# Kernel tuning notes

Measured on AMD Instinct MI355X. Metric: run time of the kernel, lower is better.

## Reference

```python
import jax, jax.numpy as jnp
import numpy as np

E = 512
H = 8
HD = E // H
EPS = 1e-5


def setup_inputs() -> dict:
    key = jax.random.key(0)
    ks = jax.random.split(key, 12)
    S, B = 2048, 4
    bound_in = float(np.sqrt(6.0 / (3 * E + E)))  # xavier_uniform for in_proj
    inp = {
        "x": jax.random.normal(ks[0], (S, B, E), dtype=jnp.float32),
        "in_proj_weight": jax.random.uniform(ks[1], (3 * E, E), minval=-bound_in, maxval=bound_in, dtype=jnp.float32),
        "in_proj_bias": jnp.zeros((3 * E,), jnp.float32),
        "out_proj_weight": jax.random.normal(ks[2], (E, E), dtype=jnp.float32) * 0.02,
        "out_proj_bias": jnp.zeros((E,), jnp.float32),
        "ln1_gamma": jnp.ones((E,), jnp.float32),
        "ln1_beta": jnp.zeros((E,), jnp.float32),
        "fc1_weight": jax.random.normal(ks[3], (4 * E, E), dtype=jnp.float32) * 0.02,
        "fc1_bias": jnp.zeros((4 * E,), jnp.float32),
        "fc2_weight": jax.random.normal(ks[4], (E, 4 * E), dtype=jnp.float32) * 0.02,
        "fc2_bias": jnp.zeros((E,), jnp.float32),
        "ln2_gamma": jnp.ones((E,), jnp.float32),
        "ln2_beta": jnp.zeros((E,), jnp.float32),
    }
    return inp


def _layer_norm(x, gamma, beta):
    mu = jnp.mean(x, axis=-1, keepdims=True)
    var = jnp.mean(jnp.square(x - mu), axis=-1, keepdims=True)
    return (x - mu) * jax.lax.rsqrt(var + EPS) * gamma + beta


def _encoder_layer(x, in_w, in_b, out_w, out_b, g1, b1, fc1_w, fc1_b, fc2_w, fc2_b, g2, b2):
    S, B, _ = x.shape
    # --- self attention (hand-rolled, full S x S scores as in original) ---
    qkv = x @ in_w.T + in_b                      # [S, B, 3E]
    q, k, v = jnp.split(qkv, 3, axis=-1)         # each [S, B, E]
    # [S, B, E] -> [B*H, S, HD]
    def to_heads(t):
        return t.reshape(S, B * H, HD).transpose(1, 0, 2)
    q, k, v = to_heads(q), to_heads(k), to_heads(v)
    scores = jnp.einsum('bsd,btd->bst', q, k) / jnp.sqrt(jnp.float32(HD))  # [B*H, S, S]
    attn_w = jax.nn.softmax(scores, axis=-1)
    attn = jnp.einsum('bst,btd->bsd', attn_w, v)  # [B*H, S, HD]
    attn = attn.transpose(1, 0, 2).reshape(S, B, E)
    attn = attn @ out_w.T + out_b
    # --- residual + LN ---
    x = _layer_norm(x + attn, g1, b1)
    # --- FFN ---
    h = jax.nn.relu(x @ fc1_w.T + fc1_b)
    h = h @ fc2_w.T + fc2_b
    return _layer_norm(x + h, g2, b2)


def reference(x, in_proj_weight, in_proj_bias, out_proj_weight, out_proj_bias,
              ln1_gamma, ln1_beta, fc1_weight, fc1_bias, fc2_weight, fc2_bias,
              ln2_gamma, ln2_beta):
    return _encoder_layer(x, in_proj_weight, in_proj_bias, out_proj_weight, out_proj_bias,
                          ln1_gamma, ln1_beta, fc1_weight, fc1_bias, fc2_weight, fc2_bias,
                          ln2_gamma, ln2_beta)
```

## Files before the change

kernel.cpp:

```cpp
#include <hip/hip_runtime.h>

typedef _Float16 half8 __attribute__((ext_vector_type(8)));
typedef float f32x4 __attribute__((ext_vector_type(4)));

static __device__ __forceinline__ f32x4 mfma16(half8 a, half8 b, f32x4 c) {
    return __builtin_amdgcn_mfma_f32_16x16x32_f16(a, b, c, 0, 0, 0);
}

__global__ void __launch_bounds__(256) f32_to_f16(const float* __restrict__ in,
                                                  _Float16* __restrict__ out, int n) {
    long i = ((long)blockIdx.x * 256 + threadIdx.x) * 8;
    if (i >= n) return;
    f32x4 v0 = *(const f32x4*)(in + i);
    f32x4 v1 = *(const f32x4*)(in + i + 4);
    half8 h;
#pragma unroll
    for (int j = 0; j < 4; j++) { h[j] = (_Float16)v0[j]; h[4 + j] = (_Float16)v1[j]; }
    *(half8*)(out + i) = h;
}

template <int MODE>
__global__ void __launch_bounds__(256) gemm_bt(const _Float16* __restrict__ A,
                                               const _Float16* __restrict__ Bw,
                                               const float* __restrict__ bias,
                                               const float* __restrict__ resid,
                                               void* __restrict__ Cout,
                                               int M, int N, int K) {
    __shared__ __align__(16) _Float16 As[128 * 32];
    __shared__ __align__(16) _Float16 Bs[128 * 32];
    const int tid = threadIdx.x;
    const int lane = tid & 63;
    const int w = tid >> 6;
    const int g = lane >> 4, l15 = lane & 15;
    const int wm = w >> 1, wn = w & 1;
    const long rowblk = (long)blockIdx.y * 128;
    const long colblk = (long)blockIdx.x * 128;

    const int srow = tid >> 2;
    const int scol = (tid & 3) * 8;
    const _Float16* Ap = A + (rowblk + srow) * (long)K + scol;
    const _Float16* Bp = Bw + (colblk + srow) * (long)K + scol;
    const long halfK = 64L * K;

    f32x4 zero = {0.f, 0.f, 0.f, 0.f};
    f32x4 acc[4][4];
#pragma unroll
    for (int i = 0; i < 4; i++)
#pragma unroll
        for (int j = 0; j < 4; j++) acc[i][j] = zero;

    for (int k0 = 0; k0 < K; k0 += 32) {
        half8 a1 = *(const half8*)(Ap + k0);
        half8 a2 = *(const half8*)(Ap + halfK + k0);
        half8 b1 = *(const half8*)(Bp + k0);
        half8 b2 = *(const half8*)(Bp + halfK + k0);
        __syncthreads();
        *(half8*)(As + tid * 8) = a1;
        *(half8*)(As + 2048 + tid * 8) = a2;
        *(half8*)(Bs + tid * 8) = b1;
        *(half8*)(Bs + 2048 + tid * 8) = b2;
        __syncthreads();
        half8 af[4], bf[4];
#pragma unroll
        for (int mi = 0; mi < 4; mi++)
            af[mi] = *(const half8*)(As + (wm * 64 + mi * 16 + l15) * 32 + g * 8);
#pragma unroll
        for (int ni = 0; ni < 4; ni++)
            bf[ni] = *(const half8*)(Bs + (wn * 64 + ni * 16 + l15) * 32 + g * 8);
#pragma unroll
        for (int mi = 0; mi < 4; mi++)
#pragma unroll
            for (int ni = 0; ni < 4; ni++)
                acc[mi][ni] = mfma16(af[mi], bf[ni], acc[mi][ni]);
    }

    const long crow0 = rowblk + wm * 64 + g * 4;
    const long ccol0 = colblk + wn * 64 + l15;
#pragma unroll
    for (int mi = 0; mi < 4; mi++) {
#pragma unroll
        for (int ni = 0; ni < 4; ni++) {
            const long cc = ccol0 + ni * 16;
            const float bv = bias[cc];
#pragma unroll
            for (int r = 0; r < 4; r++) {
                const long rr = crow0 + mi * 16 + r;
                float v = acc[mi][ni][r] + bv;
                if (MODE == 1) v = fmaxf(v, 0.f);
                if (MODE == 2) {
                    ((float*)Cout)[rr * N + cc] = v + resid[rr * N + cc];
                } else {
                    ((_Float16*)Cout)[rr * N + cc] = (_Float16)v;
                }
            }
        }
    }
}

__global__ void __launch_bounds__(256) build_vt(const _Float16* __restrict__ qkv,
                                                _Float16* __restrict__ vt) {
    const int tid = threadIdx.x, lane = tid & 63, w = tid >> 6;
    const int bh = blockIdx.y, b = bh >> 3, h = bh & 7;
    const int tc = blockIdx.x * 4 + w;
    const int d = lane;
#pragma unroll
    for (int jj = 0; jj < 8; jj++) {
        half8 buf;
#pragma unroll
        for (int j = 0; j < 8; j++) {
            int t = tc * 64 + jj * 8 + j;
            buf[j] = qkv[(long)(t * 4 + b) * 1536 + 1024 + h * 64 + d];
        }
        *(half8*)(vt + (long)(bh * 64 + d) * 2048 + tc * 64 + jj * 8) = buf;
    }
}

__global__ void __launch_bounds__(256) attn_fwd(const _Float16* __restrict__ qkv,
                                                const _Float16* __restrict__ vt,
                                                _Float16* __restrict__ attn_out) {
    __shared__ __align__(16) _Float16 Plds[4][32 * 72];
    const int tid = threadIdx.x;
    const int lane = tid & 63;
    const int w = tid >> 6;
    const int g = lane >> 4, l15 = lane & 15;
    const int bh = blockIdx.y;
    const int b = bh >> 3, h = bh & 7;
    const int s0 = blockIdx.x * 128 + w * 32;
    const int qoff = h * 64;

    half8 qa[2][2];
#pragma unroll
    for (int mi = 0; mi < 2; mi++)
#pragma unroll
        for (int ks = 0; ks < 2; ks++) {
            long row = (long)((s0 + mi * 16 + l15) * 4 + b) * 1536;
            qa[mi][ks] = *(const half8*)(qkv + row + qoff + ks * 32 + g * 8);
        }

    f32x4 zero = {0.f, 0.f, 0.f, 0.f};
    f32x4 o[2][4];
    float mst[2][4], lst[2][4];
#pragma unroll
    for (int mi = 0; mi < 2; mi++) {
#pragma unroll
        for (int di = 0; di < 4; di++) o[mi][di] = zero;
#pragma unroll
        for (int r = 0; r < 4; r++) { mst[mi][r] = -1e30f; lst[mi][r] = 0.f; }
    }

    for (int t0 = 0; t0 < 2048; t0 += 64) {
        f32x4 sa[2][4];
#pragma unroll
        for (int mi = 0; mi < 2; mi++)
#pragma unroll
            for (int ni = 0; ni < 4; ni++) sa[mi][ni] = zero;

#pragma unroll
        for (int ni = 0; ni < 4; ni++)
#pragma unroll
            for (int ks = 0; ks < 2; ks++) {
                long row = (long)((t0 + ni * 16 + l15) * 4 + b) * 1536;
                half8 kb = *(const half8*)(qkv + row + 512 + qoff + ks * 32 + g * 8);
                sa[0][ni] = mfma16(qa[0][ks], kb, sa[0][ni]);
                sa[1][ni] = mfma16(qa[1][ks], kb, sa[1][ni]);
            }

#pragma unroll
        for (int mi = 0; mi < 2; mi++)
#pragma unroll
            for (int ni = 0; ni < 4; ni++)
#pragma unroll
                for (int r = 0; r < 4; r++) sa[mi][ni][r] *= 0.125f;

        float corr[2][4];
#pragma unroll
        for (int mi = 0; mi < 2; mi++)
#pragma unroll
            for (int r = 0; r < 4; r++) {
                float mx = fmaxf(fmaxf(sa[mi][0][r], sa[mi][1][r]),
                                 fmaxf(sa[mi][2][r], sa[mi][3][r]));
                mx = fmaxf(mx, __shfl_xor(mx, 1));
                mx = fmaxf(mx, __shfl_xor(mx, 2));
                mx = fmaxf(mx, __shfl_xor(mx, 4));
                mx = fmaxf(mx, __shfl_xor(mx, 8));
                float mnew = fmaxf(mst[mi][r], mx);
                float c = __expf(mst[mi][r] - mnew);
                corr[mi][r] = c;
                mst[mi][r] = mnew;
                float rs = 0.f;
#pragma unroll
                for (int ni = 0; ni < 4; ni++) {
                    float p = __expf(sa[mi][ni][r] - mnew);
                    sa[mi][ni][r] = p;
                    rs += p;
                }
                rs += __shfl_xor(rs, 1);
                rs += __shfl_xor(rs, 2);
                rs += __shfl_xor(rs, 4);
                rs += __shfl_xor(rs, 8);
                lst[mi][r] = lst[mi][r] * c + rs;
                const int prow = mi * 16 + g * 4 + r;
#pragma unroll
                for (int ni = 0; ni < 4; ni++)
                    Plds[w][prow * 72 + ni * 16 + l15] = (_Float16)sa[mi][ni][r];
            }

#pragma unroll
        for (int mi = 0; mi < 2; mi++)
#pragma unroll
            for (int di = 0; di < 4; di++)
#pragma unroll
                for (int r = 0; r < 4; r++) o[mi][di][r] *= corr[mi][r];

        half8 pa[2][2];
#pragma unroll
        for (int mi = 0; mi < 2; mi++)
#pragma unroll
            for (int ks = 0; ks < 2; ks++)
                pa[mi][ks] = *(const half8*)&Plds[w][(mi * 16 + l15) * 72 + ks * 32 + g * 8];
#pragma unroll
        for (int di = 0; di < 4; di++)
#pragma unroll
            for (int ks = 0; ks < 2; ks++) {
                long vrow = (long)(bh * 64 + di * 16 + l15) * 2048;
                half8 vb = *(const half8*)(vt + vrow + t0 + ks * 32 + g * 8);
                o[0][di] = mfma16(pa[0][ks], vb, o[0][di]);
                o[1][di] = mfma16(pa[1][ks], vb, o[1][di]);
            }
    }

#pragma unroll
    for (int mi = 0; mi < 2; mi++)
#pragma unroll
        for (int r = 0; r < 4; r++) {
            float inv = 1.f / lst[mi][r];
            long srow = (long)((s0 + mi * 16 + g * 4 + r) * 4 + b) * 512;
#pragma unroll
            for (int di = 0; di < 4; di++)
                attn_out[srow + qoff + di * 16 + l15] = (_Float16)(o[mi][di][r] * inv);
        }
}

__global__ void __launch_bounds__(256) ln_rows(const float* __restrict__ in,
                                               const float* __restrict__ gamma,
                                               const float* __restrict__ beta,
                                               float* __restrict__ outf,
                                               _Float16* __restrict__ outh) {
    const int tid = threadIdx.x, lane = tid & 63, w = tid >> 6;
    const long row = (long)blockIdx.x * 4 + w;
    const float* p = in + row * 512 + lane * 8;
    f32x4 v0 = *(const f32x4*)p;
    f32x4 v1 = *(const f32x4*)(p + 4);
    float s = v0[0] + v0[1] + v0[2] + v0[3] + v1[0] + v1[1] + v1[2] + v1[3];
    float q = v0[0] * v0[0] + v0[1] * v0[1] + v0[2] * v0[2] + v0[3] * v0[3] +
              v1[0] * v1[0] + v1[1] * v1[1] + v1[2] * v1[2] + v1[3] * v1[3];
#pragma unroll
    for (int off = 1; off < 64; off <<= 1) {
        s += __shfl_xor(s, off);
        q += __shfl_xor(q, off);
    }
    const float mu = s * (1.0f / 512.0f);
    const float var = q * (1.0f / 512.0f) - mu * mu;
    const float rstd = rsqrtf(var + 1e-5f);
    const float* gp = gamma + lane * 8;
    const float* bp = beta + lane * 8;
    f32x4 g0 = *(const f32x4*)gp, g1 = *(const f32x4*)(gp + 4);
    f32x4 b0 = *(const f32x4*)bp, b1 = *(const f32x4*)(bp + 4);
    f32x4 o0, o1;
#pragma unroll
    for (int j = 0; j < 4; j++) {
        o0[j] = (v0[j] - mu) * rstd * g0[j] + b0[j];
        o1[j] = (v1[j] - mu) * rstd * g1[j] + b1[j];
    }
    float* op = outf + row * 512 + lane * 8;
    *(f32x4*)op = o0;
    *(f32x4*)(op + 4) = o1;
    if (outh) {
        half8 h;
#pragma unroll
        for (int j = 0; j < 4; j++) { h[j] = (_Float16)o0[j]; h[4 + j] = (_Float16)o1[j]; }
        *(half8*)(outh + row * 512 + lane * 8) = h;
    }
}

extern "C" void kernel_launch(void* const* d_in, const int* in_sizes, int n_in,
                              void* d_out, int out_size, void* d_ws, size_t ws_size,
                              hipStream_t stream) {
    const float* x    = (const float*)d_in[0];
    const float* inw  = (const float*)d_in[1];
    const float* inb  = (const float*)d_in[2];
    const float* outw = (const float*)d_in[3];
    const float* outb = (const float*)d_in[4];
    const float* g1   = (const float*)d_in[5];
    const float* b1   = (const float*)d_in[6];
    const float* f1w  = (const float*)d_in[7];
    const float* f1b  = (const float*)d_in[8];
    const float* f2w  = (const float*)d_in[9];
    const float* f2b  = (const float*)d_in[10];
    const float* g2   = (const float*)d_in[11];
    const float* b2   = (const float*)d_in[12];

    char* ws = (char*)d_ws;
    const long MB = 1024 * 1024;
    _Float16* X16  = (_Float16*)(ws + 0);
    _Float16* QKV  = (_Float16*)(ws + 8 * MB);
    _Float16* H16  = (_Float16*)(ws + 0);
    _Float16* VT   = (_Float16*)(ws + 32 * MB);
    _Float16* ATT  = (_Float16*)(ws + 40 * MB);
    float*    PRE  = (float*)(ws + 48 * MB);
    float*    YF   = (float*)(ws + 64 * MB);
    _Float16* Y16  = (_Float16*)(ws + 80 * MB);
    _Float16* WIN  = (_Float16*)(ws + 88 * MB);
    _Float16* WOUT = (_Float16*)(ws + 90 * MB);
    _Float16* WF1  = (_Float16*)(ws + 91 * MB);
    _Float16* WF2  = (_Float16*)(ws + 93 * MB);

    f32_to_f16<<<2048, 256, 0, stream>>>(x, X16, 8192 * 512);
    f32_to_f16<<<384, 256, 0, stream>>>(inw, WIN, 1536 * 512);
    f32_to_f16<<<128, 256, 0, stream>>>(outw, WOUT, 512 * 512);
    f32_to_f16<<<512, 256, 0, stream>>>(f1w, WF1, 2048 * 512);
    f32_to_f16<<<512, 256, 0, stream>>>(f2w, WF2, 512 * 2048);

    gemm_bt<0><<<dim3(12, 64), 256, 0, stream>>>(X16, WIN, inb, nullptr, QKV, 8192, 1536, 512);
    build_vt<<<dim3(8, 32), 256, 0, stream>>>(QKV, VT);
    attn_fwd<<<dim3(16, 32), 256, 0, stream>>>(QKV, VT, ATT);
    gemm_bt<2><<<dim3(4, 64), 256, 0, stream>>>(ATT, WOUT, outb, x, PRE, 8192, 512, 512);
    ln_rows<<<2048, 256, 0, stream>>>(PRE, g1, b1, YF, Y16);
    gemm_bt<1><<<dim3(16, 64), 256, 0, stream>>>(Y16, WF1, f1b, nullptr, H16, 8192, 2048, 512);
    gemm_bt<2><<<dim3(4, 64), 256, 0, stream>>>(H16, WF2, f2b, YF, PRE, 8192, 512, 2048);
    ln_rows<<<2048, 256, 0, stream>>>(PRE, g2, b2, (float*)d_out, nullptr);
}
```

Before: 360.3 us.

## Write QKV head-major, use direct-to-LDS GEMM loads, shrink attention and N=512 tiles

The QKV projection epilogue now scatters Q, K and V into contiguous per-head [B*H, S, 64] buffers. A shared-memory tiled transpose builds V^T, and attention reads contiguous head rows instead of strided 1536-wide rows. GEMM tile loads now use global_load_lds to bypass registers. A template parameter gives the N=512 GEMMs 64-wide tiles for more blocks. Attention uses 16 query rows per wave with twice as many blocks, and the softmax scale is folded into the exp. Risks are scattered 2-byte stores in the QKV epilogue and the loss of K/V register reuse across two query tiles.

```diff
diff --git a/kernel.cpp b/kernel.cpp
--- a/kernel.cpp
+++ b/kernel.cpp
@@ -5,6 +5,13 @@
 
 static __device__ __forceinline__ f32x4 mfma16(half8 a, half8 b, f32x4 c) {
     return __builtin_amdgcn_mfma_f32_16x16x32_f16(a, b, c, 0, 0, 0);
+}
+
+static __device__ __forceinline__ void gload16(const void* g, const void* l) {
+    __builtin_amdgcn_global_load_lds(
+        (const __attribute__((address_space(1))) unsigned int*)(unsigned long long)g,
+        (__attribute__((address_space(3))) unsigned int*)(unsigned int)(unsigned long long)l,
+        16, 0, 0);
 }
 
 __global__ void __launch_bounds__(256) f32_to_f16(const float* __restrict__ in,
@@ -19,67 +26,63 @@
     *(half8*)(out + i) = h;
 }
 
-template <int MODE>
+template <int MODE, int NI>
 __global__ void __launch_bounds__(256) gemm_bt(const _Float16* __restrict__ A,
                                                const _Float16* __restrict__ Bw,
                                                const float* __restrict__ bias,
                                                const float* __restrict__ resid,
                                                void* __restrict__ Cout,
                                                int M, int N, int K) {
+    constexpr int BN = 32 * NI;
     __shared__ __align__(16) _Float16 As[128 * 32];
-    __shared__ __align__(16) _Float16 Bs[128 * 32];
+    __shared__ __align__(16) _Float16 Bs[BN * 32];
     const int tid = threadIdx.x;
     const int lane = tid & 63;
     const int w = tid >> 6;
     const int g = lane >> 4, l15 = lane & 15;
     const int wm = w >> 1, wn = w & 1;
     const long rowblk = (long)blockIdx.y * 128;
-    const long colblk = (long)blockIdx.x * 128;
-
-    const int srow = tid >> 2;
-    const int scol = (tid & 3) * 8;
-    const _Float16* Ap = A + (rowblk + srow) * (long)K + scol;
-    const _Float16* Bp = Bw + (colblk + srow) * (long)K + scol;
-    const long halfK = 64L * K;
+    const long colblk = (long)blockIdx.x * BN;
+
+    const int lrow = lane >> 2;
+    const int lcol = (lane & 3) * 8;
 
     f32x4 zero = {0.f, 0.f, 0.f, 0.f};
-    f32x4 acc[4][4];
+    f32x4 acc[4][NI];
 #pragma unroll
     for (int i = 0; i < 4; i++)
 #pragma unroll
-        for (int j = 0; j < 4; j++) acc[i][j] = zero;
+        for (int j = 0; j < NI; j++) acc[i][j] = zero;
 
     for (int k0 = 0; k0 < K; k0 += 32) {
-        half8 a1 = *(const half8*)(Ap + k0);
-        half8 a2 = *(const half8*)(Ap + halfK + k0);
-        half8 b1 = *(const half8*)(Bp + k0);
-        half8 b2 = *(const half8*)(Bp + halfK + k0);
         __syncthreads();
-        *(half8*)(As + tid * 8) = a1;
-        *(half8*)(As + 2048 + tid * 8) = a2;
-        *(half8*)(Bs + tid * 8) = b1;
-        *(half8*)(Bs + 2048 + tid * 8) = b2;
+        gload16(A + (rowblk + w * 32 + lrow) * (long)K + k0 + lcol, As + w * 1024);
+        gload16(A + (rowblk + w * 32 + 16 + lrow) * (long)K + k0 + lcol, As + w * 1024 + 512);
+#pragma unroll
+        for (int c = 0; c < NI / 2; c++)
+            gload16(Bw + (colblk + w * (8 * NI) + c * 16 + lrow) * (long)K + k0 + lcol,
+                    Bs + w * (8 * NI) * 32 + c * 512);
         __syncthreads();
-        half8 af[4], bf[4];
+        half8 af[4], bf[NI];
 #pragma unroll
         for (int mi = 0; mi < 4; mi++)
             af[mi] = *(const half8*)(As + (wm * 64 + mi * 16 + l15) * 32 + g * 8);
 #pragma unroll
-        for (int ni = 0; ni < 4; ni++)
-            bf[ni] = *(const half8*)(Bs + (wn * 64 + ni * 16 + l15) * 32 + g * 8);
+        for (int ni = 0; ni < NI; ni++)
+            bf[ni] = *(const half8*)(Bs + (wn * (16 * NI) + ni * 16 + l15) * 32 + g * 8);
 #pragma unroll
         for (int mi = 0; mi < 4; mi++)
 #pragma unroll
-            for (int ni = 0; ni < 4; ni++)
+            for (int ni = 0; ni < NI; ni++)
                 acc[mi][ni] = mfma16(af[mi], bf[ni], acc[mi][ni]);
     }
 
     const long crow0 = rowblk + wm * 64 + g * 4;
-    const long ccol0 = colblk + wn * 64 + l15;
+    const long ccol0 = colblk + wn * (16 * NI) + l15;
 #pragma unroll
     for (int mi = 0; mi < 4; mi++) {
 #pragma unroll
-        for (int ni = 0; ni < 4; ni++) {
+        for (int ni = 0; ni < NI; ni++) {
             const long cc = ccol0 + ni * 16;
             const float bv = bias[cc];
 #pragma unroll
@@ -89,6 +92,13 @@
                 if (MODE == 1) v = fmaxf(v, 0.f);
                 if (MODE == 2) {
                     ((float*)Cout)[rr * N + cc] = v + resid[rr * N + cc];
+                } else if (MODE == 3) {
+                    const long sel = cc >> 9;
+                    const int hh = (int)(cc >> 6) & 7;
+                    const int dd = (int)cc & 63;
+                    const int ss = (int)(rr >> 2), bb = (int)rr & 3;
+                    ((_Float16*)Cout)[sel * (32L * 2048 * 64) +
+                                      ((long)(bb * 8 + hh) * 2048 + ss) * 64 + dd] = (_Float16)v;
                 } else {
                     ((_Float16*)Cout)[rr * N + cc] = (_Float16)v;
                 }
@@ -97,148 +107,122 @@
     }
 }
 
-__global__ void __launch_bounds__(256) build_vt(const _Float16* __restrict__ qkv,
-                                                _Float16* __restrict__ vt) {
-    const int tid = threadIdx.x, lane = tid & 63, w = tid >> 6;
-    const int bh = blockIdx.y, b = bh >> 3, h = bh & 7;
-    const int tc = blockIdx.x * 4 + w;
-    const int d = lane;
-#pragma unroll
-    for (int jj = 0; jj < 8; jj++) {
-        half8 buf;
-#pragma unroll
-        for (int j = 0; j < 8; j++) {
-            int t = tc * 64 + jj * 8 + j;
-            buf[j] = qkv[(long)(t * 4 + b) * 1536 + 1024 + h * 64 + d];
-        }
-        *(half8*)(vt + (long)(bh * 64 + d) * 2048 + tc * 64 + jj * 8) = buf;
-    }
-}
-
-__global__ void __launch_bounds__(256) attn_fwd(const _Float16* __restrict__ qkv,
-                                                const _Float16* __restrict__ vt,
-                                                _Float16* __restrict__ attn_out) {
-    __shared__ __align__(16) _Float16 Plds[4][32 * 72];
+__global__ void __launch_bounds__(256) transpose_v(const _Float16* __restrict__ Vh,
+                                                   _Float16* __restrict__ Vt) {
+    __shared__ _Float16 T[64][72];
+    const int tid = threadIdx.x;
+    const int bh = blockIdx.y;
+    const int t0 = blockIdx.x * 64;
+    const _Float16* src = Vh + ((long)bh * 2048 + t0) * 64;
+    const int row = tid >> 2, col = (tid & 3) * 16;
+    *(half8*)&T[row][col] = *(const half8*)(src + row * 64 + col);
+    *(half8*)&T[row][col + 8] = *(const half8*)(src + row * 64 + col + 8);
+    __syncthreads();
+    const int d = tid >> 2, tc = (tid & 3) * 16;
+    half8 a, b;
+#pragma unroll
+    for (int j = 0; j < 8; j++) { a[j] = T[tc + j][d]; b[j] = T[tc + 8 + j][d]; }
+    _Float16* dst = Vt + ((long)bh * 64 + d) * 2048 + t0 + tc;
+    *(half8*)dst = a;
+    *(half8*)(dst + 8) = b;
+}
+
+__global__ void __launch_bounds__(256) attn_fwd(const _Float16* __restrict__ Qh,
+                                                const _Float16* __restrict__ Kh,
+                                                const _Float16* __restrict__ Vt,
+                                                _Float16* __restrict__ out) {
+    __shared__ __align__(16) _Float16 Plds[4][16 * 72];
     const int tid = threadIdx.x;
     const int lane = tid & 63;
     const int w = tid >> 6;
     const int g = lane >> 4, l15 = lane & 15;
     const int bh = blockIdx.y;
     const int b = bh >> 3, h = bh & 7;
-    const int s0 = blockIdx.x * 128 + w * 32;
-    const int qoff = h * 64;
-
-    half8 qa[2][2];
-#pragma unroll
-    for (int mi = 0; mi < 2; mi++)
-#pragma unroll
-        for (int ks = 0; ks < 2; ks++) {
-            long row = (long)((s0 + mi * 16 + l15) * 4 + b) * 1536;
-            qa[mi][ks] = *(const half8*)(qkv + row + qoff + ks * 32 + g * 8);
+    const int s0 = blockIdx.x * 64 + w * 16;
+    const _Float16* Qb = Qh + (long)bh * 2048 * 64;
+    const _Float16* Kb = Kh + (long)bh * 2048 * 64;
+    const _Float16* Vb = Vt + (long)bh * 64 * 2048;
+
+    half8 qa[2];
+#pragma unroll
+    for (int ks = 0; ks < 2; ks++)
+        qa[ks] = *(const half8*)(Qb + (s0 + l15) * 64 + ks * 32 + g * 8);
+
+    f32x4 zero = {0.f, 0.f, 0.f, 0.f};
+    f32x4 o[4];
+    float mst[4], lst[4];
+#pragma unroll
+    for (int di = 0; di < 4; di++) o[di] = zero;
+#pragma unroll
+    for (int r = 0; r < 4; r++) { mst[r] = -1e30f; lst[r] = 0.f; }
+
+    for (int t0 = 0; t0 < 2048; t0 += 64) {
+        f32x4 sa[4];
+#pragma unroll
+        for (int ni = 0; ni < 4; ni++) sa[ni] = zero;
+#pragma unroll
+        for (int ni = 0; ni < 4; ni++)
+#pragma unroll
+            for (int ks = 0; ks < 2; ks++) {
+                half8 kb = *(const half8*)(Kb + (t0 + ni * 16 + l15) * 64 + ks * 32 + g * 8);
+                sa[ni] = mfma16(qa[ks], kb, sa[ni]);
+            }
+
+        float corr[4];
+#pragma unroll
+        for (int r = 0; r < 4; r++) {
+            float mx = fmaxf(fmaxf(sa[0][r], sa[1][r]), fmaxf(sa[2][r], sa[3][r]));
+            mx = fmaxf(mx, __shfl_xor(mx, 1));
+            mx = fmaxf(mx, __shfl_xor(mx, 2));
+            mx = fmaxf(mx, __shfl_xor(mx, 4));
+            mx = fmaxf(mx, __shfl_xor(mx, 8));
+            const float mnew = fmaxf(mst[r], mx);
+            corr[r] = __expf((mst[r] - mnew) * 0.125f);
+            mst[r] = mnew;
+            float rs = 0.f;
+            float pv[4];
+#pragma unroll
+            for (int ni = 0; ni < 4; ni++) {
+                pv[ni] = __expf((sa[ni][r] - mnew) * 0.125f);
+                rs += pv[ni];
+            }
+            rs += __shfl_xor(rs, 1);
+            rs += __shfl_xor(rs, 2);
+            rs += __shfl_xor(rs, 4);
+            rs += __shfl_xor(rs, 8);
+            lst[r] = lst[r] * corr[r] + rs;
+            const int prow = g * 4 + r;
+#pragma unroll
+            for (int ni = 0; ni < 4; ni++)
+                Plds[w][prow * 72 + ni * 16 + l15] = (_Float16)pv[ni];
         }
 
-    f32x4 zero = {0.f, 0.f, 0.f, 0.f};
-    f32x4 o[2][4];
-    float mst[2][4], lst[2][4];
-#pragma unroll
-    for (int mi = 0; mi < 2; mi++) {
-#pragma unroll
-        for (int di = 0; di < 4; di++) o[mi][di] = zero;
-#pragma unroll
-        for (int r = 0; r < 4; r++) { mst[mi][r] = -1e30f; lst[mi][r] = 0.f; }
-    }
-
-    for (int t0 = 0; t0 < 2048; t0 += 64) {
-        f32x4 sa[2][4];
-#pragma unroll
-        for (int mi = 0; mi < 2; mi++)
-#pragma unroll
-            for (int ni = 0; ni < 4; ni++) sa[mi][ni] = zero;
-
-#pragma unroll
-        for (int ni = 0; ni < 4; ni++)
+#pragma unroll
+        for (int di = 0; di < 4; di++)
+#pragma unroll
+            for (int r = 0; r < 4; r++) o[di][r] *= corr[r];
+
+        half8 pa[2];
+#pragma unroll
+        for (int ks = 0; ks < 2; ks++)
+            pa[ks] = *(const half8*)&Plds[w][l15 * 72 + ks * 32 + g * 8];
+#pragma unroll
+        for (int di = 0; di < 4; di++)
 #pragma unroll
             for (int ks = 0; ks < 2; ks++) {
-                long row = (long)((t0 + ni * 16 + l15) * 4 + b) * 1536;
-                half8 kb = *(const half8*)(qkv + row + 512 + qoff + ks * 32 + g * 8);
-                sa[0][ni] = mfma16(qa[0][ks], kb, sa[0][ni]);
-                sa[1][ni] = mfma16(qa[1][ks], kb, sa[1][ni]);
+                half8 vb = *(const half8*)(Vb + (di * 16 + l15) * 2048 + t0 + ks * 32 + g * 8);
+                o[di] = mfma16(pa[ks], vb, o[di]);
             }
-
-#pragma unroll
-        for (int mi = 0; mi < 2; mi++)
-#pragma unroll
-            for (int ni = 0; ni < 4; ni++)
-#pragma unroll
-                for (int r = 0; r < 4; r++) sa[mi][ni][r] *= 0.125f;
-
-        float corr[2][4];
-#pragma unroll
-        for (int mi = 0; mi < 2; mi++)
-#pragma unroll
-            for (int r = 0; r < 4; r++) {
-                float mx = fmaxf(fmaxf(sa[mi][0][r], sa[mi][1][r]),
-                                 fmaxf(sa[mi][2][r], sa[mi][3][r]));
-                mx = fmaxf(mx, __shfl_xor(mx, 1));
-                mx = fmaxf(mx, __shfl_xor(mx, 2));
-                mx = fmaxf(mx, __shfl_xor(mx, 4));
-                mx = fmaxf(mx, __shfl_xor(mx, 8));
-                float mnew = fmaxf(mst[mi][r], mx);
-                float c = __expf(mst[mi][r] - mnew);
-                corr[mi][r] = c;
-                mst[mi][r] = mnew;
-                float rs = 0.f;
-#pragma unroll
-                for (int ni = 0; ni < 4; ni++) {
-                    float p = __expf(sa[mi][ni][r] - mnew);
-                    sa[mi][ni][r] = p;
-                    rs += p;
-                }
-                rs += __shfl_xor(rs, 1);
-                rs += __shfl_xor(rs, 2);
-                rs += __shfl_xor(rs, 4);
-                rs += __shfl_xor(rs, 8);
-                lst[mi][r] = lst[mi][r] * c + rs;
-                const int prow = mi * 16 + g * 4 + r;
-#pragma unroll
-                for (int ni = 0; ni < 4; ni++)
-                    Plds[w][prow * 72 + ni * 16 + l15] = (_Float16)sa[mi][ni][r];
-            }
-
-#pragma unroll
-        for (int mi = 0; mi < 2; mi++)
-#pragma unroll
-            for (int di = 0; di < 4; di++)
-#pragma unroll
-                for (int r = 0; r < 4; r++) o[mi][di][r] *= corr[mi][r];
-
-        half8 pa[2][2];
-#pragma unroll
-        for (int mi = 0; mi < 2; mi++)
-#pragma unroll
-            for (int ks = 0; ks < 2; ks++)
-                pa[mi][ks] = *(const half8*)&Plds[w][(mi * 16 + l15) * 72 + ks * 32 + g * 8];
+    }
+
+#pragma unroll
+    for (int r = 0; r < 4; r++) {
+        const float inv = 1.f / lst[r];
+        const long srow = (long)((s0 + g * 4 + r) * 4 + b) * 512;
 #pragma unroll
         for (int di = 0; di < 4; di++)
-#pragma unroll
-            for (int ks = 0; ks < 2; ks++) {
-                long vrow = (long)(bh * 64 + di * 16 + l15) * 2048;
-                half8 vb = *(const half8*)(vt + vrow + t0 + ks * 32 + g * 8);
-                o[0][di] = mfma16(pa[0][ks], vb, o[0][di]);
-                o[1][di] = mfma16(pa[1][ks], vb, o[1][di]);
-            }
-    }
-
-#pragma unroll
-    for (int mi = 0; mi < 2; mi++)
-#pragma unroll
-        for (int r = 0; r < 4; r++) {
-            float inv = 1.f / lst[mi][r];
-            long srow = (long)((s0 + mi * 16 + g * 4 + r) * 4 + b) * 512;
-#pragma unroll
-            for (int di = 0; di < 4; di++)
-                attn_out[srow + qoff + di * 16 + l15] = (_Float16)(o[mi][di][r] * inv);
-        }
+            out[srow + h * 64 + di * 16 + l15] = (_Float16)(o[di][r] * inv);
+    }
 }
 
 __global__ void __launch_bounds__(256) ln_rows(const float* __restrict__ in,
@@ -276,10 +260,10 @@
     *(f32x4*)op = o0;
     *(f32x4*)(op + 4) = o1;
     if (outh) {
-        half8 h;
-#pragma unroll
-        for (int j = 0; j < 4; j++) { h[j] = (_Float16)o0[j]; h[4 + j] = (_Float16)o1[j]; }
-        *(half8*)(outh + row * 512 + lane * 8) = h;
+        half8 hh;
+#pragma unroll
+        for (int j = 0; j < 4; j++) { hh[j] = (_Float16)o0[j]; hh[4 + j] = (_Float16)o1[j]; }
+        *(half8*)(outh + row * 512 + lane * 8) = hh;
     }
 }
 
@@ -302,18 +286,22 @@
 
     char* ws = (char*)d_ws;
     const long MB = 1024 * 1024;
-    _Float16* X16  = (_Float16*)(ws + 0);
-    _Float16* QKV  = (_Float16*)(ws + 8 * MB);
-    _Float16* H16  = (_Float16*)(ws + 0);
-    _Float16* VT   = (_Float16*)(ws + 32 * MB);
-    _Float16* ATT  = (_Float16*)(ws + 40 * MB);
-    float*    PRE  = (float*)(ws + 48 * MB);
-    float*    YF   = (float*)(ws + 64 * MB);
-    _Float16* Y16  = (_Float16*)(ws + 80 * MB);
-    _Float16* WIN  = (_Float16*)(ws + 88 * MB);
-    _Float16* WOUT = (_Float16*)(ws + 90 * MB);
-    _Float16* WF1  = (_Float16*)(ws + 91 * MB);
-    _Float16* WF2  = (_Float16*)(ws + 93 * MB);
+    _Float16* X16   = (_Float16*)(ws + 0);
+    _Float16* HEADS = (_Float16*)(ws + 8 * MB);
+    _Float16* H16   = (_Float16*)(ws + 0);
+    _Float16* VT    = (_Float16*)(ws + 32 * MB);
+    _Float16* ATT   = (_Float16*)(ws + 40 * MB);
+    float*    PRE   = (float*)(ws + 48 * MB);
+    float*    YF    = (float*)(ws + 64 * MB);
+    _Float16* Y16   = (_Float16*)(ws + 80 * MB);
+    _Float16* WIN   = (_Float16*)(ws + 88 * MB);
+    _Float16* WOUT  = (_Float16*)(ws + 90 * MB);
+    _Float16* WF1   = (_Float16*)(ws + 91 * MB);
+    _Float16* WF2   = (_Float16*)(ws + 93 * MB);
+
+    _Float16* Qh = HEADS;
+    _Float16* Kh = HEADS + 32L * 2048 * 64;
+    _Float16* Vh = HEADS + 2 * 32L * 2048 * 64;
 
     f32_to_f16<<<2048, 256, 0, stream>>>(x, X16, 8192 * 512);
     f32_to_f16<<<384, 256, 0, stream>>>(inw, WIN, 1536 * 512);
@@ -321,12 +309,12 @@
     f32_to_f16<<<512, 256, 0, stream>>>(f1w, WF1, 2048 * 512);
     f32_to_f16<<<512, 256, 0, stream>>>(f2w, WF2, 512 * 2048);
 
-    gemm_bt<0><<<dim3(12, 64), 256, 0, stream>>>(X16, WIN, inb, nullptr, QKV, 8192, 1536, 512);
-    build_vt<<<dim3(8, 32), 256, 0, stream>>>(QKV, VT);
-    attn_fwd<<<dim3(16, 32), 256, 0, stream>>>(QKV, VT, ATT);
-    gemm_bt<2><<<dim3(4, 64), 256, 0, stream>>>(ATT, WOUT, outb, x, PRE, 8192, 512, 512);
+    gemm_bt<3, 4><<<dim3(12, 64), 256, 0, stream>>>(X16, WIN, inb, nullptr, HEADS, 8192, 1536, 512);
+    transpose_v<<<dim3(32, 32), 256, 0, stream>>>(Vh, VT);
+    attn_fwd<<<dim3(32, 32), 256, 0, stream>>>(Qh, Kh, VT, ATT);
+    gemm_bt<2, 2><<<dim3(8, 64), 256, 0, stream>>>(ATT, WOUT, outb, x, PRE, 8192, 512, 512);
     ln_rows<<<2048, 256, 0, stream>>>(PRE, g1, b1, YF, Y16);
-    gemm_bt<1><<<dim3(16, 64), 256, 0, stream>>>(Y16, WF1, f1b, nullptr, H16, 8192, 2048, 512);
-    gemm_bt<2><<<dim3(4, 64), 256, 0, stream>>>(H16, WF2, f2b, YF, PRE, 8192, 512, 2048);
+    gemm_bt<1, 4><<<dim3(16, 64), 256, 0, stream>>>(Y16, WF1, f1b, nullptr, H16, 8192, 2048, 512);
+    gemm_bt<2, 2><<<dim3(8, 64), 256, 0, stream>>>(H16, WF2, f2b, YF, PRE, 8192, 512, 2048);
     ln_rows<<<2048, 256, 0, stream>>>(PRE, g2, b2, (float*)d_out, nullptr);
 }
```

Result: slower. 476.0 us (+32.1%).
